# Kernel optimization log

Measured on AMD Instinct MI355X. Metric: run time of the kernel, lower is better.

The kernel has to match this reference:

```python
import jax, jax.numpy as jnp
import numpy as np

B, T, E, H, NH, L, R, K, N, P, HOR = 32, 16, 768, 1024, 16, 6, 8, 16, 100000, 9, 8
HD = H // NH


def _ln(x, g, b):
    m = jnp.mean(x, -1, keepdims=True)
    v = jnp.mean((x - m) ** 2, -1, keepdims=True)
    return (x - m) * jax.lax.rsqrt(v + 1e-5) * g + b


def _lora(x, W, A, Bm, b):
    # base linear + low-rank update: x W^T + (x A^T) B^T + b
    return x @ W.T + (x @ A.T) @ Bm.T + b


def setup_inputs() -> dict:
    key = jax.random.key(0)
    ks = iter(jax.random.split(key, 64))
    def rn(shape, s):
        return jax.random.normal(next(ks), shape, dtype=jnp.float32) * s
    d = {}
    d['history_img_emb'] = rn((B, T, E), 1.0)
    d['current_emb'] = rn((B, E), 1.0)
    d['goal_emb'] = rn((B, E), 1.0)
    d['subgoal_emb'] = rn((B, E), 1.0)
    d['beacon_emb'] = rn((B, E), 1.0)
    d['history_proprio'] = rn((B, T, P), 1.0)
    d['proprio'] = rn((B, P), 1.0)
    d['bank'] = rn((N, E), 1.0)
    d['hp_W'] = rn((H, E + P), 0.02); d['hp_b'] = jnp.zeros((H,), jnp.float32)
    d['ip_W'] = rn((H, E), 0.02); d['ip_b'] = jnp.zeros((H,), jnp.float32)
    d['pp_W'] = rn((H, P), 0.02); d['pp_b'] = jnp.zeros((H,), jnp.float32)
    d['plan_token'] = rn((1, 1, H), 0.02)
    d['ln1_g'] = jnp.ones((L, H), jnp.float32); d['ln1_b'] = jnp.zeros((L, H), jnp.float32)
    d['ln2_g'] = jnp.ones((L, H), jnp.float32); d['ln2_b'] = jnp.zeros((L, H), jnp.float32)
    for nm, o, i in (('q', H, H), ('k', H, H), ('v', H, H), ('o', H, H), ('f1', 4 * H, H), ('f2', H, 4 * H)):
        d[nm + 'W'] = rn((L, o, i), 0.02)
        d[nm + 'A'] = rn((L, R, i), 0.02)
        d[nm + 'B'] = rn((L, o, R), 0.02)
        d[nm + 'b'] = jnp.zeros((L, o), jnp.float32)
    d['fln_g'] = jnp.ones((H,), jnp.float32); d['fln_b'] = jnp.zeros((H,), jnp.float32)
    d['ah_W1'] = rn((H, H), 0.02); d['ah_b1'] = jnp.zeros((H,), jnp.float32)
    d['ah_W2'] = rn((3, H), 0.02); d['ah_b2'] = jnp.zeros((3,), jnp.float32)
    d['rh_W1'] = rn((H, H + 3), 0.02); d['rh_b1'] = jnp.zeros((H,), jnp.float32)
    d['rh_W2'] = rn((HOR * 3, H), 0.02); d['rh_b2'] = jnp.zeros((HOR * 3,), jnp.float32)
    d['sh_W'] = rn((1, H), 0.02); d['sh_b'] = jnp.zeros((1,), jnp.float32)
    return d


def reference(history_img_emb, current_emb, goal_emb, subgoal_emb, beacon_emb,
              history_proprio, proprio, bank,
              hp_W, hp_b, ip_W, ip_b, pp_W, pp_b, plan_token,
              ln1_g, ln1_b, ln2_g, ln2_b,
              qW, qA, qB, qb, kW, kA, kB, kb, vW, vA, vB, vb, oW, oA, oB, ob,
              f1W, f1A, f1B, f1b, f2W, f2A, f2B, f2b,
              fln_g, fln_b, ah_W1, ah_b1, ah_W2, ah_b2,
              rh_W1, rh_b1, rh_W2, rh_b2, sh_W, sh_b):
    # batched semantic-bank top-k retrieval (replaces the per-sample python loop)
    sims = current_emb @ bank.T                      # [B, N]
    scores, idx = jax.lax.top_k(sims, K)             # [B, K]
    sem = bank[idx] * scores[..., None]              # [B, K, E] gather + scale

    # multi-modal token fusion
    hist = jnp.concatenate([history_img_emb, history_proprio], -1) @ hp_W.T + hp_b  # [B, T, H]
    img = lambda e: e @ ip_W.T + ip_b
    goal_t = img(goal_emb)[:, None]
    sub_t = img(subgoal_emb)[:, None]
    bea_t = img(beacon_emb)[:, None]
    sem_t = img(sem)                                 # [B, K, H]
    prop_t = (proprio @ pp_W.T + pp_b)[:, None]
    plan_t = jnp.broadcast_to(plan_token, (B, 1, H))
    x = jnp.concatenate([plan_t, hist, goal_t, sub_t, bea_t, sem_t, prop_t], 1)  # [B, S=37, H]

    scale = 1.0 / np.sqrt(HD).astype(np.float32)
    for l in range(L):
        h = _ln(x, ln1_g[l], ln1_b[l])
        q = _lora(h, qW[l], qA[l], qB[l], qb[l]).reshape(B, -1, NH, HD)
        k = _lora(h, kW[l], kA[l], kB[l], kb[l]).reshape(B, -1, NH, HD)
        v = _lora(h, vW[l], vA[l], vB[l], vb[l]).reshape(B, -1, NH, HD)
        attn = jax.nn.softmax(jnp.einsum('bshd,bthd->bhst', q, k) * scale, axis=-1)
        out = jnp.einsum('bhst,bthd->bshd', attn, v).reshape(B, -1, H)
        x = x + _lora(out, oW[l], oA[l], oB[l], ob[l])
        h2 = _ln(x, ln2_g[l], ln2_b[l])
        x = x + _lora(jax.nn.gelu(_lora(h2, f1W[l], f1A[l], f1B[l], f1b[l]), approximate=False),
                      f2W[l], f2A[l], f2B[l], f2b[l])

    x = _ln(x, fln_g, fln_b)
    ps = x[:, 0]                                     # plan token state [B, H]
    anchor = jax.nn.gelu(ps @ ah_W1.T + ah_b1, approximate=False) @ ah_W2.T + ah_b2  # [B, 3]
    ref_in = jnp.concatenate([ps, anchor], -1)
    waypoints = (jax.nn.gelu(ref_in @ rh_W1.T + rh_b1, approximate=False) @ rh_W2.T + rh_b2).reshape(B, HOR, 3)
    stop_logit = (ps @ sh_W.T + sh_b)[:, 0]          # [B]
    return anchor, waypoints, stop_logit
```

## Files before the change

### kernel.cpp

```cpp
#include <hip/hip_runtime.h>
#include <float.h>
#include <math.h>

#define NB 100000
#define SEQ 37
#define NTOK 1184
#define TKCH 16

typedef __attribute__((ext_vector_type(8))) short short8;
typedef __attribute__((ext_vector_type(4))) float floatx4;

__device__ __forceinline__ short f2bf(float f) {
  union { float f; unsigned u; } x; x.f = f;
  unsigned r = x.u + 0x7fff + ((x.u >> 16) & 1);
  return (short)(r >> 16);
}

__device__ __forceinline__ float gelu_f(float v) {
  return 0.5f * v * (1.f + erff(v * 0.70710678118654752f));
}

__global__ __launch_bounds__(256) void wconv_all(const float* __restrict__ qW,
                                                 const float* __restrict__ kW,
                                                 const float* __restrict__ vW,
                                                 const float* __restrict__ oW,
                                                 const float* __restrict__ f1W,
                                                 const float* __restrict__ f2W,
                                                 short* __restrict__ wb) {
  const int l = blockIdx.x / 1536;
  const int t = blockIdx.x - l * 1536;
  const float* src; int Kd; size_t doff; int np, kc;
  if (t < 512) {
    const int w = t >> 7, ti = t & 127;
    const float* base = (w == 0) ? qW : (w == 1) ? kW : (w == 2) ? vW : oW;
    src = base + (size_t)l * 1024 * 1024;
    Kd = 1024; np = ti >> 4; kc = ti & 15;
    doff = (size_t)w * 1048576 + ((size_t)np * 16 + kc) * 8192;
  } else if (t < 1024) {
    const int ti = t - 512;
    src = f1W + (size_t)l * 4096 * 1024;
    Kd = 1024; np = ti >> 4; kc = ti & 15;
    doff = (size_t)4 * 1048576 + ((size_t)np * 16 + kc) * 8192;
  } else {
    const int ti = t - 1024;
    src = f2W + (size_t)l * 1024 * 4096;
    Kd = 4096; np = ti >> 6; kc = ti & 63;
    doff = (size_t)8 * 1048576 + ((size_t)np * 64 + kc) * 8192;
  }
  short* dst = wb + (size_t)l * 12 * 1048576 + doff;
  const float* sp = src + (size_t)(np * 128) * Kd + kc * 64;
  const int tid = threadIdx.x;
#pragma unroll
  for (int q = 0; q < 4; ++q) {
    const int d = q * 256 + tid;
    const int row = d >> 3, slot = d & 7;
    const int ss = slot ^ (row & 7);
    const float* s = sp + (size_t)row * Kd + ss * 8;
    const float4 u0 = *(const float4*)s;
    const float4 u1 = *(const float4*)(s + 4);
    short8 v;
    v[0] = f2bf(u0.x); v[1] = f2bf(u0.y); v[2] = f2bf(u0.z); v[3] = f2bf(u0.w);
    v[4] = f2bf(u1.x); v[5] = f2bf(u1.y); v[6] = f2bf(u1.z); v[7] = f2bf(u1.w);
    *(short8*)(dst + (size_t)d * 8) = v;
  }
}

__global__ __launch_bounds__(256) void wconv_embed(const float* __restrict__ hpW,
                                                   const float* __restrict__ ipW,
                                                   short* __restrict__ wbe) {
  const int t = blockIdx.x;
  const float* src; int Kd, np, kc; size_t doff;
  if (t < 104) { src = hpW; Kd = 777; np = t / 13; kc = t - np * 13; doff = (size_t)t * 8192; }
  else { const int ti = t - 104; src = ipW; Kd = 768; np = ti / 12; kc = ti - np * 12;
         doff = (size_t)t * 8192; }
  short* dst = wbe + doff;
  const int tid = threadIdx.x;
#pragma unroll
  for (int q = 0; q < 4; ++q) {
    const int d = q * 256 + tid;
    const int row = d >> 3, slot = d & 7;
    const int ss = slot ^ (row & 7);
    const int gk0 = kc * 64 + ss * 8;
    const float* s = src + (size_t)(np * 128 + row) * Kd;
    short8 v;
#pragma unroll
    for (int e = 0; e < 8; ++e) v[e] = (gk0 + e < Kd) ? f2bf(s[gk0 + e]) : (short)0;
    *(short8*)(dst + (size_t)d * 8) = v;
  }
}

__global__ __launch_bounds__(256) void gemm_bt(const float* __restrict__ A, int lda,
                                               const short* __restrict__ WT, size_t wzstride,
                                               const float* __restrict__ b0,
                                               const float* __restrict__ b1,
                                               const float* __restrict__ b2,
                                               const float* __restrict__ LT,
                                               const float* __restrict__ B0,
                                               const float* __restrict__ B1,
                                               const float* __restrict__ B2,
                                               float* __restrict__ C, size_t czstride,
                                               int ldc, int M, int K,
                                               int acc_flag, int gelu_flag,
                                               int ksn, float* __restrict__ part) {
  __shared__ short Al[2][64 * 64];
  __shared__ short Wl[2][128 * 64];
  const int z = blockIdx.z;
  const int kidx = (ksn > 1) ? z : 0;
  const float* bias = (ksn > 1 || z == 0) ? b0 : (z == 1) ? b1 : b2;
  const float* Bz = (ksn > 1 || z == 0) ? B0 : (z == 1) ? B1 : B2;
  if (ksn == 1) C += (size_t)z * czstride;
  const int nkc_tot = K >> 6;
  const int nkc = nkc_tot / ksn;
  const short* wt = WT + (size_t)((ksn > 1) ? 0 : z) * wzstride +
                    ((size_t)blockIdx.y * nkc_tot + (size_t)kidx * nkc) * 8192;
  const int tid = threadIdx.x;
  const int wid = tid >> 6, lane = tid & 63;
  const int wr = wid >> 1, wc = wid & 1;
  const int bm = blockIdx.x * 64, bn = blockIdx.y * 128;
  const int arow = tid >> 2;
  const int s0 = (tid & 3) * 2;

  floatx4 acc[2][4];
#pragma unroll
  for (int i = 0; i < 2; ++i)
#pragma unroll
    for (int j = 0; j < 4; ++j)
#pragma unroll
      for (int r = 0; r < 4; ++r) acc[i][j][r] = 0.f;

  const int ga = bm + arow;
  const bool aok = ga < M;
  const float* ap = A + (size_t)ga * lda + (size_t)kidx * nkc * 64;
  const int aswz = arow & 7;

  float4 ar[4];
  short8 wreg[4];

#define LOAD_A(kc_)                                                        \
  {                                                                        \
    _Pragma("unroll") for (int j = 0; j < 2; ++j) {                        \
      const int slot = s0 + j;                                             \
      if (aok) {                                                           \
        ar[j * 2] = *(const float4*)(ap + (kc_)*64 + slot * 8);            \
        ar[j * 2 + 1] = *(const float4*)(ap + (kc_)*64 + slot * 8 + 4);    \
      } else {                                                             \
        ar[j * 2] = make_float4(0.f, 0.f, 0.f, 0.f);                      \
        ar[j * 2 + 1] = make_float4(0.f, 0.f, 0.f, 0.f);                  \
      }                                                                    \
    }                                                                      \
  }
#define LOAD_W(kc_)                                                        \
  {                                                                        \
    _Pragma("unroll") for (int it = 0; it < 4; ++it)                       \
        wreg[it] = *(const short8*)(wt + (size_t)(kc_)*8192 + (it * 256 + tid) * 8); \
  }
#define WRITE_A(buf_)                                                      \
  {                                                                        \
    _Pragma("unroll") for (int j = 0; j < 2; ++j) {                        \
      const int slot = s0 + j;                                             \
      short8 s;                                                            \
      s[0] = f2bf(ar[j * 2].x); s[1] = f2bf(ar[j * 2].y);                  \
      s[2] = f2bf(ar[j * 2].z); s[3] = f2bf(ar[j * 2].w);                  \
      s[4] = f2bf(ar[j * 2 + 1].x); s[5] = f2bf(ar[j * 2 + 1].y);          \
      s[6] = f2bf(ar[j * 2 + 1].z); s[7] = f2bf(ar[j * 2 + 1].w);          \
      *(short8*)&Al[buf_][arow * 64 + ((slot ^ aswz) << 3)] = s;           \
    }                                                                      \
  }
#define WRITE_W(buf_)                                                      \
  {                                                                        \
    _Pragma("unroll") for (int it = 0; it < 4; ++it)                       \
        *(short8*)&Wl[buf_][(it * 256 + tid) * 8] = wreg[it];              \
  }

  LOAD_W(0) LOAD_A(0)
  WRITE_A(0) WRITE_W(0)
  __syncthreads();

  for (int t = 0; t < nkc; ++t) {
    const int cur = t & 1, nxt = cur ^ 1;
    const bool more = (t + 1 < nkc);
    if (more) { LOAD_W(t + 1) LOAD_A(t + 1) }
#pragma unroll
    for (int ks = 0; ks < 2; ++ks) {
      short8 af[2], wf[4];
#pragma unroll
      for (int i = 0; i < 2; ++i) {
        const int row = wr * 32 + i * 16 + (lane & 15);
        const int sa = (ks * 4 + (lane >> 4)) ^ (row & 7);
        af[i] = *(const short8*)&Al[cur][row * 64 + sa * 8];
      }
#pragma unroll
      for (int j = 0; j < 4; ++j) {
        const int col = wc * 64 + j * 16 + (lane & 15);
        const int sw2 = (ks * 4 + (lane >> 4)) ^ (col & 7);
        wf[j] = *(const short8*)&Wl[cur][col * 64 + sw2 * 8];
      }
#pragma unroll
      for (int i = 0; i < 2; ++i)
#pragma unroll
        for (int j = 0; j < 4; ++j)
          acc[i][j] = __builtin_amdgcn_mfma_f32_16x16x32_bf16(af[i], wf[j], acc[i][j], 0, 0, 0);
    }
    if (more) { WRITE_A(nxt) WRITE_W(nxt) }
    __syncthreads();
  }
#undef LOAD_A
#undef LOAD_W
#undef WRITE_A
#undef WRITE_W

  if (ksn > 1) {
#pragma unroll
    for (int i = 0; i < 2; ++i) {
      const int gm0 = bm + wr * 32 + i * 16 + (lane >> 4) * 4;
#pragma unroll
      for (int r = 0; r < 4; ++r) {
        const int gm = gm0 + r;
        if (gm >= M) continue;
#pragma unroll
        for (int j = 0; j < 4; ++j) {
          const int gn = bn + wc * 64 + j * 16 + (lane & 15);
          part[((size_t)kidx * M + gm) * ldc + gn] = acc[i][j][r];
        }
      }
    }
    return;
  }

  float br[4][8];
  if (LT) {
#pragma unroll
    for (int j = 0; j < 4; ++j) {
      const int gn = bn + wc * 64 + j * 16 + (lane & 15);
      const float4 u0 = *(const float4*)(Bz + (size_t)gn * 8);
      const float4 u1 = *(const float4*)(Bz + (size_t)gn * 8 + 4);
      br[j][0] = u0.x; br[j][1] = u0.y; br[j][2] = u0.z; br[j][3] = u0.w;
      br[j][4] = u1.x; br[j][5] = u1.y; br[j][6] = u1.z; br[j][7] = u1.w;
    }
  }
#pragma unroll
  for (int i = 0; i < 2; ++i) {
    const int gm0 = bm + wr * 32 + i * 16 + (lane >> 4) * 4;
#pragma unroll
    for (int r = 0; r < 4; ++r) {
      const int gm = gm0 + r;
      if (gm >= M) continue;
      float lt[8];
      if (LT) {
        const float4 t0 = *(const float4*)(LT + ((size_t)z * NTOK + gm) * 8);
        const float4 t1 = *(const float4*)(LT + ((size_t)z * NTOK + gm) * 8 + 4);
        lt[0] = t0.x; lt[1] = t0.y; lt[2] = t0.z; lt[3] = t0.w;
        lt[4] = t1.x; lt[5] = t1.y; lt[6] = t1.z; lt[7] = t1.w;
      }
#pragma unroll
      for (int j = 0; j < 4; ++j) {
        const int gn = bn + wc * 64 + j * 16 + (lane & 15);
        float o = acc[i][j][r] + bias[gn];
        if (LT)
          o += lt[0] * br[j][0] + lt[1] * br[j][1] + lt[2] * br[j][2] + lt[3] * br[j][3] +
               lt[4] * br[j][4] + lt[5] * br[j][5] + lt[6] * br[j][6] + lt[7] * br[j][7];
        const size_t off = (size_t)gm * ldc + gn;
        if (acc_flag) o += C[off];
        if (gelu_flag) o = gelu_f(o);
        C[off] = o;
      }
    }
  }
}

__global__ __launch_bounds__(256) void reduce_ks(const float* __restrict__ part,
                                                 const float* __restrict__ bias,
                                                 const float* __restrict__ LT,
                                                 const float* __restrict__ Bm,
                                                 float* __restrict__ X, int KS) {
  const int idx = blockIdx.x * 256 + threadIdx.x;
  if (idx >= NTOK * 1024) return;
  const int gm = idx >> 10, gn = idx & 1023;
  float s = 0.f;
  for (int h = 0; h < KS; ++h) s += part[(size_t)h * NTOK * 1024 + idx];
  const float* t = LT + (size_t)gm * 8;
  const float* bp = Bm + (size_t)gn * 8;
  s += t[0] * bp[0] + t[1] * bp[1] + t[2] * bp[2] + t[3] * bp[3] +
       t[4] * bp[4] + t[5] * bp[5] + t[6] * bp[6] + t[7] * bp[7];
  X[idx] += s + bias[gn];
}

__global__ __launch_bounds__(256) void gemm_sm2(const float* __restrict__ A, int lda,
                                                const float* __restrict__ W, int ldw,
                                                const float* __restrict__ bias,
                                                float* __restrict__ C, int ldc,
                                                float* __restrict__ part,
                                                int N, int K, int gelu_flag) {
  __shared__ float buf[8192];
  const int tid = threadIdx.x;
  const int col = tid >> 3, ksub = tid & 7;
  const int gcol = blockIdx.x * 32 + col;
  const int KS = gridDim.y, ky = blockIdx.y;
  const int kchunk = (((K + KS - 1) / KS) + 127) & ~127;
  const int kstart = ky * kchunk;
  const int kend = (kstart + kchunk < K) ? (kstart + kchunk) : K;
  const float* wp = W + (size_t)(gcol < N ? gcol : 0) * ldw;

  float acc[32];
#pragma unroll
  for (int m = 0; m < 32; ++m) acc[m] = 0.f;

  for (int kc = kstart; kc < kend; kc += 128) {
    __syncthreads();
#pragma unroll
    for (int q = 0; q < 4; ++q) {
      const int idx4 = q * 256 + tid;
      const int m = idx4 >> 5, j = (idx4 & 31) * 4;
      const int gk = kc + j;
      float4 v;
      if (gk + 3 < K) {
        v = *(const float4*)(A + (size_t)m * lda + gk);
      } else {
        v.x = (gk < K) ? A[(size_t)m * lda + gk] : 0.f;
        v.y = (gk + 1 < K) ? A[(size_t)m * lda + gk + 1] : 0.f;
        v.z = (gk + 2 < K) ? A[(size_t)m * lda + gk + 2] : 0.f;
        v.w = (gk + 3 < K) ? A[(size_t)m * lda + gk + 3] : 0.f;
      }
      *(float4*)&buf[m * 128 + j] = v;
    }
    __syncthreads();
#pragma unroll
    for (int kk = 0; kk < 4; ++kk) {
      const int j = kk * 32 + ksub * 4;
      const int gk = kc + j;
      float4 w4 = make_float4(0.f, 0.f, 0.f, 0.f);
      if (gcol < N && gk < K) {
        if (gk + 3 < K) {
          w4 = *(const float4*)(wp + gk);
        } else {
          w4.x = wp[gk];
          if (gk + 1 < K) w4.y = wp[gk + 1];
          if (gk + 2 < K) w4.z = wp[gk + 2];
        }
      }
#pragma unroll
      for (int m = 0; m < 32; ++m) {
        const float4 a4 = *(const float4*)&buf[m * 128 + j];
        acc[m] += a4.x * w4.x + a4.y * w4.y + a4.z * w4.z + a4.w * w4.w;
      }
    }
  }
  __syncthreads();
#pragma unroll
  for (int m = 0; m < 32; ++m) buf[m * 256 + ksub * 32 + col] = acc[m];
  __syncthreads();
#pragma unroll
  for (int g = 0; g < 4; ++g) {
    const int idx = g * 256 + tid;
    const int m = idx >> 5, c = idx & 31;
    float s = 0.f;
#pragma unroll
    for (int h = 0; h < 8; ++h) s += buf[m * 256 + h * 32 + c];
    const int gc = blockIdx.x * 32 + c;
    if (gc < N) {
      if (KS == 1) {
        float o = s + bias[gc];
        if (gelu_flag) o = gelu_f(o);
        C[(size_t)m * ldc + gc] = o;
      } else {
        part[((size_t)ky * 32 + m) * N + gc] = s;
      }
    }
  }
}

__global__ __launch_bounds__(256) void reduce_sm(const float* __restrict__ part,
                                                 const float* __restrict__ bias,
                                                 float* __restrict__ C, int ldc,
                                                 int N, int KS, int gelu_flag) {
  const int idx = blockIdx.x * 256 + threadIdx.x;
  if (idx >= 32 * N) return;
  const int m = idx / N, c = idx - m * N;
  float s = 0.f;
  for (int h = 0; h < KS; ++h) s += part[((size_t)h * 32 + m) * N + c];
  float o = s + bias[c];
  if (gelu_flag) o = gelu_f(o);
  C[(size_t)m * ldc + c] = o;
}

__global__ __launch_bounds__(256) void sims_kernel(const float* __restrict__ cur,
                                                   const float* __restrict__ bank,
                                                   float* __restrict__ sims) {
  __shared__ float Bs[32][132];
  __shared__ float Cs[32][36];
  const int tid = threadIdx.x;
  const int tx = tid & 7;
  const int ty = tid >> 3;
  const int n0 = blockIdx.x * 128;
  const int srow = tid >> 1;
  const int spart = tid & 1;
  const int cb = tid >> 3;
  const int ck = (tid & 7) * 4;

  float acc[4][4] = {{0.f,0.f,0.f,0.f},{0.f,0.f,0.f,0.f},
                     {0.f,0.f,0.f,0.f},{0.f,0.f,0.f,0.f}};

  const bool rok = (n0 + srow) < NB;
  const float* bp = bank + (size_t)(n0 + srow) * 768 + spart * 16;
  const float* cp = cur + (size_t)cb * 768 + ck;

  for (int kc = 0; kc < 768; kc += 32) {
    __syncthreads();
#pragma unroll
    for (int jj = 0; jj < 4; ++jj) {
      float4 v = rok ? *(const float4*)(bp + kc + jj * 4)
                     : make_float4(0.f, 0.f, 0.f, 0.f);
      const int kk = spart * 16 + jj * 4;
      Bs[kk + 0][srow] = v.x; Bs[kk + 1][srow] = v.y;
      Bs[kk + 2][srow] = v.z; Bs[kk + 3][srow] = v.w;
    }
    {
      float4 v = *(const float4*)(cp + kc);
      Cs[ck + 0][cb] = v.x; Cs[ck + 1][cb] = v.y;
      Cs[ck + 2][cb] = v.z; Cs[ck + 3][cb] = v.w;
    }
    __syncthreads();
#pragma unroll
    for (int kk = 0; kk < 32; ++kk) {
      float4 av = *(const float4*)&Bs[kk][ty * 4];
      float4 bv = *(const float4*)&Cs[kk][tx * 4];
      float a4[4] = {av.x, av.y, av.z, av.w};
      float b4[4] = {bv.x, bv.y, bv.z, bv.w};
#pragma unroll
      for (int i = 0; i < 4; ++i)
#pragma unroll
        for (int j = 0; j < 4; ++j) acc[i][j] += a4[i] * b4[j];
    }
  }
  const int n = n0 + ty * 4;
#pragma unroll
  for (int j = 0; j < 4; ++j) {
    const int b = tx * 4 + j;
    float4 o = make_float4(acc[0][j], acc[1][j], acc[2][j], acc[3][j]);
    if (n + 3 < NB) {
      *(float4*)(sims + (size_t)b * NB + n) = o;
    } else {
      float oo[4] = {o.x, o.y, o.z, o.w};
      for (int i = 0; i < 4; ++i)
        if (n + i < NB) sims[(size_t)b * NB + n + i] = oo[i];
    }
  }
}

__global__ __launch_bounds__(256) void topk_stage1(const float* __restrict__ sims,
                                                   float* __restrict__ cv,
                                                   int* __restrict__ ci) {
  __shared__ float ss[4096];
  __shared__ int si[4096];
  __shared__ float wv[4];
  __shared__ int wi[4];
  const int chunk = blockIdx.x, b = blockIdx.y, tid = threadIdx.x;
  const int start = chunk * (NB / TKCH), end = start + (NB / TKCH);
  float ls[16]; int li[16];
#pragma unroll
  for (int i = 0; i < 16; ++i) { ls[i] = -FLT_MAX; li[i] = 0x7fffffff; }
  const float* row = sims + (size_t)b * NB;
  float lmin = -FLT_MAX;
  for (int n = start + tid; n < end; n += 256) {
    float v = row[n];
    if (v > lmin) {
      int p = 15;
      while (p > 0 && ls[p - 1] < v) { ls[p] = ls[p - 1]; li[p] = li[p - 1]; --p; }
      ls[p] = v; li[p] = n;
      lmin = ls[15];
    }
  }
#pragma unroll
  for (int i = 0; i < 16; ++i) { ss[i * 256 + tid] = ls[i]; si[i * 256 + tid] = li[i]; }
  __syncthreads();
  for (int round = 0; round < 16; ++round) {
    float bv = -FLT_MAX; int bi = 0x7fffffff;
#pragma unroll
    for (int i = 0; i < 16; ++i) {
      float v = ss[i * 256 + tid]; int ix = si[i * 256 + tid];
      if (v > bv || (v == bv && ix < bi)) { bv = v; bi = ix; }
    }
#pragma unroll
    for (int s = 32; s; s >>= 1) {
      float ov = __shfl_down(bv, s); int oi = __shfl_down(bi, s);
      if (ov > bv || (ov == bv && oi < bi)) { bv = ov; bi = oi; }
    }
    if ((tid & 63) == 0) { wv[tid >> 6] = bv; wi[tid >> 6] = bi; }
    __syncthreads();
    if (tid == 0) {
      bv = wv[0]; bi = wi[0];
      for (int w = 1; w < 4; ++w)
        if (wv[w] > bv || (wv[w] == bv && wi[w] < bi)) { bv = wv[w]; bi = wi[w]; }
      cv[(b * TKCH + chunk) * 16 + round] = bv;
      ci[(b * TKCH + chunk) * 16 + round] = bi;
      wi[0] = bi;
    }
    __syncthreads();
    bi = wi[0];
#pragma unroll
    for (int i = 0; i < 16; ++i)
      if (si[i * 256 + tid] == bi) ss[i * 256 + tid] = -FLT_MAX;
    __syncthreads();
  }
}

__global__ __launch_bounds__(256) void topk_stage2(const float* __restrict__ cv,
                                                   const int* __restrict__ ci,
                                                   float* __restrict__ tks,
                                                   int* __restrict__ tki) {
  __shared__ float wv[4];
  __shared__ int wi[4];
  __shared__ int bw;
  const int b = blockIdx.x, tid = threadIdx.x;
  float val = cv[b * 256 + tid];
  int idx = ci[b * 256 + tid];
  for (int round = 0; round < 16; ++round) {
    float bv = val; int bi = idx;
#pragma unroll
    for (int s = 1; s < 64; s <<= 1) {
      float ov = __shfl_xor(bv, s); int oi = __shfl_xor(bi, s);
      if (ov > bv || (ov == bv && oi < bi)) { bv = ov; bi = oi; }
    }
    if ((tid & 63) == 0) { wv[tid >> 6] = bv; wi[tid >> 6] = bi; }
    __syncthreads();
    if (tid == 0) {
      bv = wv[0]; bi = wi[0];
      for (int w = 1; w < 4; ++w)
        if (wv[w] > bv || (wv[w] == bv && wi[w] < bi)) { bv = wv[w]; bi = wi[w]; }
      tks[b * 16 + round] = bv; tki[b * 16 + round] = bi;
      bw = bi;
    }
    __syncthreads();
    if (idx == bw) val = -FLT_MAX;
  }
}

__global__ void sem_kernel(const float* __restrict__ bank, const float* __restrict__ tks,
                           const int* __restrict__ tki, float* __restrict__ sem) {
  int slot = blockIdx.x;
  float s = tks[slot]; int idx = tki[slot];
  for (int i = threadIdx.x; i < 768; i += 256)
    sem[(size_t)slot * 768 + i] = bank[(size_t)idx * 768 + i] * s;
}

__global__ void build_hist_in(const float* __restrict__ img, const float* __restrict__ pr,
                              float* __restrict__ out) {
  int r = blockIdx.x;
  for (int i = threadIdx.x; i < 832; i += 256)
    out[(size_t)r * 832 + i] = (i < 768) ? img[(size_t)r * 768 + i]
                             : (i < 777) ? pr[r * 9 + (i - 768)] : 0.f;
}

__global__ void build_img_in(const float* __restrict__ goal, const float* __restrict__ sub,
                             const float* __restrict__ bea, const float* __restrict__ sem,
                             float* __restrict__ out) {
  int r = blockIdx.x;
  const float* src = (r < 32) ? goal + (size_t)r * 768
                   : (r < 64) ? sub + (size_t)(r - 32) * 768
                   : (r < 96) ? bea + (size_t)(r - 64) * 768
                              : sem + (size_t)(r - 96) * 768;
  for (int i = threadIdx.x; i < 768; i += 256) out[(size_t)r * 768 + i] = src[i];
}

__global__ void assemble_x(const float* __restrict__ th, const float* __restrict__ ti,
                           const float* __restrict__ tp, const float* __restrict__ plan,
                           float* __restrict__ x) {
  int r = blockIdx.x;
  int b = r / SEQ, tok = r - b * SEQ;
  const float* src;
  if (tok == 0) src = plan;
  else if (tok <= 16) src = th + (size_t)(b * 16 + tok - 1) * 1024;
  else if (tok <= 19) src = ti + (size_t)((tok - 17) * 32 + b) * 1024;
  else if (tok <= 35) src = ti + (size_t)(96 + b * 16 + (tok - 20)) * 1024;
  else src = tp + (size_t)b * 1024;
  for (int i = threadIdx.x; i < 1024; i += 256) x[(size_t)r * 1024 + i] = src[i];
}

__global__ void build_ref(const float* __restrict__ ps, const float* __restrict__ anc,
                          float* __restrict__ ref) {
  int b = blockIdx.x;
  for (int i = threadIdx.x; i < 1027; i += 256)
    ref[(size_t)b * 1027 + i] = (i < 1024) ? ps[(size_t)b * 1024 + i] : anc[b * 3 + (i - 1024)];
}

__device__ __forceinline__ float block_sum256(float v, float* red) {
#pragma unroll
  for (int s = 32; s; s >>= 1) v += __shfl_down(v, s);
  if ((threadIdx.x & 63) == 0) red[threadIdx.x >> 6] = v;
  __syncthreads();
  float tot = red[0] + red[1] + red[2] + red[3];
  __syncthreads();
  return tot;
}

__global__ __launch_bounds__(256) void ln_kernel(const float* __restrict__ in, int in_stride,
                                                 float* __restrict__ out,
                                                 const float* __restrict__ g,
                                                 const float* __restrict__ bt) {
  __shared__ float red[4];
  const float* xr = in + (size_t)blockIdx.x * in_stride;
  const int tid = threadIdx.x;
  float v[4];
#pragma unroll
  for (int i = 0; i < 4; ++i) v[i] = xr[tid + 256 * i];
  float mean = block_sum256(v[0] + v[1] + v[2] + v[3], red) * (1.f / 1024.f);
  float sq = 0.f;
#pragma unroll
  for (int i = 0; i < 4; ++i) { float d = v[i] - mean; sq += d * d; }
  float var = block_sum256(sq, red) * (1.f / 1024.f);
  float inv = rsqrtf(var + 1e-5f);
  float* orow = out + (size_t)blockIdx.x * 1024;
#pragma unroll
  for (int i = 0; i < 4; ++i) {
    int c = tid + 256 * i;
    orow[c] = (v[i] - mean) * inv * g[c] + bt[c];
  }
}

__global__ __launch_bounds__(256) void lora_down(const float* __restrict__ h,
                                                 const float* __restrict__ A0,
                                                 const float* __restrict__ A1,
                                                 const float* __restrict__ A2,
                                                 float* __restrict__ lt, int K) {
  __shared__ float red[4][8];
  const int m = blockIdx.x, z = blockIdx.y;
  const int tid = threadIdx.x, wave = tid >> 6, lane = tid & 63;
  const float* A = (z == 0) ? A0 : (z == 1) ? A1 : A2;
  float p[8] = {0.f, 0.f, 0.f, 0.f, 0.f, 0.f, 0.f, 0.f};
  for (int kk = tid; kk < K; kk += 256) {
    float hv = h[(size_t)m * K + kk];
#pragma unroll
    for (int r = 0; r < 8; ++r) p[r] += hv * A[r * K + kk];
  }
#pragma unroll
  for (int s = 1; s < 64; s <<= 1) {
#pragma unroll
    for (int r = 0; r < 8; ++r) p[r] += __shfl_xor(p[r], s);
  }
  if (lane == 0) {
#pragma unroll
    for (int r = 0; r < 8; ++r) red[wave][r] = p[r];
  }
  __syncthreads();
  if (tid < 8)
    lt[((size_t)z * NTOK + m) * 8 + tid] =
        red[0][tid] + red[1][tid] + red[2][tid] + red[3][tid];
}

__global__ __launch_bounds__(256) void attn_kernel(const float* __restrict__ q,
                                                   const float* __restrict__ k,
                                                   const float* __restrict__ v,
                                                   float* __restrict__ ao) {
  __shared__ float qs[SEQ * 64], ks[SEQ * 64], vs[SEQ * 64], sc[SEQ * 40];
  const int head = blockIdx.x, b = blockIdx.y, tid = threadIdx.x;
  const size_t base = ((size_t)b * SEQ) * 1024 + head * 64;
  for (int i = tid; i < SEQ * 64; i += 256) {
    int s = i >> 6, d = i & 63;
    size_t off = base + (size_t)s * 1024 + d;
    qs[i] = q[off]; ks[i] = k[off]; vs[i] = v[off];
  }
  __syncthreads();
  for (int p = tid; p < SEQ * SEQ; p += 256) {
    int s = p / SEQ, t = p - s * SEQ;
    float acc = 0.f;
#pragma unroll 16
    for (int d = 0; d < 64; ++d) acc += qs[s * 64 + d] * ks[t * 64 + d];
    sc[s * 40 + t] = acc * 0.125f;
  }
  __syncthreads();
  if (tid < SEQ) {
    float m = -FLT_MAX;
    for (int t = 0; t < SEQ; ++t) m = fmaxf(m, sc[tid * 40 + t]);
    float sum = 0.f;
    for (int t = 0; t < SEQ; ++t) { float e = expf(sc[tid * 40 + t] - m); sc[tid * 40 + t] = e; sum += e; }
    float inv = 1.f / sum;
    for (int t = 0; t < SEQ; ++t) sc[tid * 40 + t] *= inv;
  }
  __syncthreads();
  for (int i = tid; i < SEQ * 64; i += 256) {
    int s = i >> 6, d = i & 63;
    float acc = 0.f;
    for (int t = 0; t < SEQ; ++t) acc += sc[s * 40 + t] * vs[t * 64 + d];
    ao[base + (size_t)s * 1024 + d] = acc;
  }
}

extern "C" void kernel_launch(void* const* d_in, const int* in_sizes, int n_in,
                              void* d_out, int out_size, void* d_ws, size_t ws_size,
                              hipStream_t stream) {
  const float* hist_img = (const float*)d_in[0];
  const float* cur      = (const float*)d_in[1];
  const float* goal     = (const float*)d_in[2];
  const float* sub      = (const float*)d_in[3];
  const float* bea      = (const float*)d_in[4];
  const float* hist_pr  = (const float*)d_in[5];
  const float* prop     = (const float*)d_in[6];
  const float* bank     = (const float*)d_in[7];
  const float* hpW = (const float*)d_in[8];  const float* hpb = (const float*)d_in[9];
  const float* ipW = (const float*)d_in[10]; const float* ipb = (const float*)d_in[11];
  const float* ppW = (const float*)d_in[12]; const float* ppb = (const float*)d_in[13];
  const float* plan = (const float*)d_in[14];
  const float* ln1g = (const float*)d_in[15]; const float* ln1b = (const float*)d_in[16];
  const float* ln2g = (const float*)d_in[17]; const float* ln2b = (const float*)d_in[18];
  const float* qW = (const float*)d_in[19]; const float* qA = (const float*)d_in[20];
  const float* qB = (const float*)d_in[21]; const float* qb = (const float*)d_in[22];
  const float* kW = (const float*)d_in[23]; const float* kA = (const float*)d_in[24];
  const float* kB = (const float*)d_in[25]; const float* kb = (const float*)d_in[26];
  const float* vW = (const float*)d_in[27]; const float* vA = (const float*)d_in[28];
  const float* vB = (const float*)d_in[29]; const float* vb = (const float*)d_in[30];
  const float* oW = (const float*)d_in[31]; const float* oA = (const float*)d_in[32];
  const float* oB = (const float*)d_in[33]; const float* ob = (const float*)d_in[34];
  const float* f1W = (const float*)d_in[35]; const float* f1A = (const float*)d_in[36];
  const float* f1B = (const float*)d_in[37]; const float* f1b = (const float*)d_in[38];
  const float* f2W = (const float*)d_in[39]; const float* f2A = (const float*)d_in[40];
  const float* f2B = (const float*)d_in[41]; const float* f2b = (const float*)d_in[42];
  const float* flng = (const float*)d_in[43]; const float* flnb = (const float*)d_in[44];
  const float* ahW1 = (const float*)d_in[45]; const float* ahb1 = (const float*)d_in[46];
  const float* ahW2 = (const float*)d_in[47]; const float* ahb2 = (const float*)d_in[48];
  const float* rhW1 = (const float*)d_in[49]; const float* rhb1 = (const float*)d_in[50];
  const float* rhW2 = (const float*)d_in[51]; const float* rhb2 = (const float*)d_in[52];
  const float* shW = (const float*)d_in[53]; const float* shb = (const float*)d_in[54];
  float* out = (float*)d_out;

  float* ws  = (float*)d_ws;
  float* F1O = ws;
  float* SIMS = ws;
  float* X   = F1O + (size_t)NTOK * 4096;
  float* Hb  = X  + (size_t)NTOK * 1024;
  float* Qb  = Hb + (size_t)NTOK * 1024;
  float* Kb  = Qb + (size_t)NTOK * 1024;
  float* Vb  = Kb + (size_t)NTOK * 1024;
  float* AOb = Vb + (size_t)NTOK * 1024;
  float* LT  = AOb + (size_t)NTOK * 1024;
  float* SEM = LT + (size_t)3 * NTOK * 8;
  float* HIN = SEM + (size_t)512 * 768;
  float* TKS = HIN + (size_t)512 * 832;
  int*   TKI = (int*)(TKS + 512);
  float* PS  = TKS + 1024;
  float* HH  = PS + 32 * 1024;
  float* REF = HH + 32 * 1024;
  float* CV  = REF + 32 * 1027;
  int*   CI  = (int*)(CV + 32 * 256);
  float* PART = (float*)(CI + 32 * 256);
  float* PF2 = PART + 8 * 32 * 1024;
  short* WB  = (short*)(PF2 + (size_t)4 * NTOK * 1024);
  short* WBE = WB + (size_t)6 * 12 * 1048576;

  const size_t czs = (size_t)NTOK * 1024;
  const size_t WM = 1048576;
  const size_t WL = 12 * WM;

  auto gemms = [&](const float* A, int lda, const float* W, int ldw, const float* bias,
                   float* C, int ldc, int N, int K, int geluf, int KS) {
    gemm_sm2<<<dim3((N + 31) / 32, KS), 256, 0, stream>>>(A, lda, W, ldw, bias,
                                                          C, ldc, PART, N, K, geluf);
    if (KS > 1)
      reduce_sm<<<(32 * N + 255) / 256, 256, 0, stream>>>(PART, bias, C, ldc, N, KS, geluf);
  };

  wconv_all<<<6 * 1536, 256, 0, stream>>>(qW, kW, vW, oW, f1W, f2W, WB);
  wconv_embed<<<200, 256, 0, stream>>>(hpW, ipW, WBE);

  sims_kernel<<<(NB + 127) / 128, 256, 0, stream>>>(cur, bank, SIMS);
  topk_stage1<<<dim3(TKCH, 32), 256, 0, stream>>>(SIMS, CV, CI);
  topk_stage2<<<32, 256, 0, stream>>>(CV, CI, TKS, TKI);
  sem_kernel<<<512, 256, 0, stream>>>(bank, TKS, TKI, SEM);

  build_hist_in<<<512, 256, 0, stream>>>(hist_img, hist_pr, HIN);
  build_img_in<<<608, 256, 0, stream>>>(goal, sub, bea, SEM, AOb);
  gemm_bt<<<dim3(8, 8, 1), 256, 0, stream>>>(
      HIN, 832, WBE, 0, hpb, hpb, hpb,
      nullptr, nullptr, nullptr, nullptr, Qb, 0, 1024, 512, 832, 0, 0, 1, nullptr);
  gemm_bt<<<dim3(10, 8, 1), 256, 0, stream>>>(
      AOb, 768, WBE + (size_t)104 * 8192, 0, ipb, ipb, ipb,
      nullptr, nullptr, nullptr, nullptr, Kb, 0, 1024, 608, 768, 0, 0, 1, nullptr);
  gemms(prop, 9, ppW, 9, ppb, Vb, 1024, 1024, 9, 0, 1);
  assemble_x<<<NTOK, 256, 0, stream>>>(Qb, Kb, Vb, plan, X);

  const int mblk = (NTOK + 63) / 64;
  for (int l = 0; l < 6; ++l) {
    const size_t aO = (size_t)l * 8 * 1024, bO = (size_t)l * 1024 * 8,
                 biO = (size_t)l * 1024;
    const size_t a4O = (size_t)l * 8 * 4096, b4O = (size_t)l * 4096 * 8,
                 bi4O = (size_t)l * 4096;
    const short* WBl = WB + (size_t)l * WL;
    ln_kernel<<<NTOK, 256, 0, stream>>>(X, 1024, Hb, ln1g + biO, ln1b + biO);
    lora_down<<<dim3(NTOK, 3), 256, 0, stream>>>(Hb, qA + aO, kA + aO, vA + aO, LT, 1024);
    gemm_bt<<<dim3(mblk, 8, 3), 256, 0, stream>>>(
        Hb, 1024, WBl, WM, qb + biO, kb + biO, vb + biO,
        LT, qB + bO, kB + bO, vB + bO, Qb, czs, 1024, NTOK, 1024, 0, 0, 1, nullptr);
    attn_kernel<<<dim3(16, 32), 256, 0, stream>>>(Qb, Kb, Vb, AOb);
    lora_down<<<dim3(NTOK, 1), 256, 0, stream>>>(AOb, oA + aO, oA + aO, oA + aO, LT, 1024);
    gemm_bt<<<dim3(mblk, 8, 2), 256, 0, stream>>>(
        AOb, 1024, WBl + 3 * WM, 0, ob + biO, ob + biO, ob + biO,
        nullptr, nullptr, nullptr, nullptr, nullptr, 0, 1024, NTOK, 1024, 0, 0, 2, PF2);
    reduce_ks<<<(NTOK * 1024 + 255) / 256, 256, 0, stream>>>(PF2, ob + biO, LT,
                                                             oB + bO, X, 2);
    ln_kernel<<<NTOK, 256, 0, stream>>>(X, 1024, Hb, ln2g + biO, ln2b + biO);
    lora_down<<<dim3(NTOK, 1), 256, 0, stream>>>(Hb, f1A + aO, f1A + aO, f1A + aO, LT, 1024);
    gemm_bt<<<dim3(mblk, 32, 1), 256, 0, stream>>>(
        Hb, 1024, WBl + 4 * WM, 0, f1b + bi4O, f1b + bi4O, f1b + bi4O,
        LT, f1B + b4O, f1B + b4O, f1B + b4O, F1O, 0, 4096, NTOK, 1024, 0, 1, 1, nullptr);
    lora_down<<<dim3(NTOK, 1), 256, 0, stream>>>(F1O, f2A + a4O, f2A + a4O, f2A + a4O, LT, 4096);
    gemm_bt<<<dim3(mblk, 8, 4), 256, 0, stream>>>(
        F1O, 4096, WBl + 8 * WM, 0, f2b + biO, f2b + biO, f2b + biO,
        nullptr, nullptr, nullptr, nullptr, nullptr, 0, 1024, NTOK, 4096, 0, 0, 4, PF2);
    reduce_ks<<<(NTOK * 1024 + 255) / 256, 256, 0, stream>>>(PF2, f2b + biO, LT,
                                                             f2B + bO, X, 4);
  }

  ln_kernel<<<32, 256, 0, stream>>>(X, SEQ * 1024, PS, flng, flnb);
  gemms(PS, 1024, ahW1, 1024, ahb1, HH, 1024, 1024, 1024, 1, 8);
  gemms(HH, 1024, ahW2, 1024, ahb2, out, 3, 3, 1024, 0, 8);
  build_ref<<<32, 256, 0, stream>>>(PS, out, REF);
  gemms(REF, 1027, rhW1, 1027, rhb1, HH, 1024, 1024, 1027, 1, 8);
  gemms(HH, 1024, rhW2, 1024, rhb2, out + 96, 24, 24, 1024, 0, 8);
  gemms(PS, 1024, shW, 1024, shb, out + 864, 1, 1, 1024, 0, 8);
}
```

Measured before the change: 1.725 ms.

## Convert weights to bf16 inside GEMM loads and fuse LoRA-down into layernorm

Removes the separate weight pre-conversion kernels. The GEMM now loads fp32 weights directly, converts them to bf16 and writes them swizzled into shared memory, which avoids one full read and write pass over all layer weights per call. The LoRA down-projections for q/k/v and f1 are also computed inside the layernorm kernel, removing two lora_down launches per layer and a reread of the normalized activations. In exchange, the GEMM reads twice as many weight bytes per tile and does the conversion work on the critical path inside the main loop.

```diff
diff --git a/kernel.cpp b/kernel.cpp
--- a/kernel.cpp
+++ b/kernel.cpp
@@ -20,77 +20,11 @@
   return 0.5f * v * (1.f + erff(v * 0.70710678118654752f));
 }
 
-__global__ __launch_bounds__(256) void wconv_all(const float* __restrict__ qW,
-                                                 const float* __restrict__ kW,
-                                                 const float* __restrict__ vW,
-                                                 const float* __restrict__ oW,
-                                                 const float* __restrict__ f1W,
-                                                 const float* __restrict__ f2W,
-                                                 short* __restrict__ wb) {
-  const int l = blockIdx.x / 1536;
-  const int t = blockIdx.x - l * 1536;
-  const float* src; int Kd; size_t doff; int np, kc;
-  if (t < 512) {
-    const int w = t >> 7, ti = t & 127;
-    const float* base = (w == 0) ? qW : (w == 1) ? kW : (w == 2) ? vW : oW;
-    src = base + (size_t)l * 1024 * 1024;
-    Kd = 1024; np = ti >> 4; kc = ti & 15;
-    doff = (size_t)w * 1048576 + ((size_t)np * 16 + kc) * 8192;
-  } else if (t < 1024) {
-    const int ti = t - 512;
-    src = f1W + (size_t)l * 4096 * 1024;
-    Kd = 1024; np = ti >> 4; kc = ti & 15;
-    doff = (size_t)4 * 1048576 + ((size_t)np * 16 + kc) * 8192;
-  } else {
-    const int ti = t - 1024;
-    src = f2W + (size_t)l * 1024 * 4096;
-    Kd = 4096; np = ti >> 6; kc = ti & 63;
-    doff = (size_t)8 * 1048576 + ((size_t)np * 64 + kc) * 8192;
-  }
-  short* dst = wb + (size_t)l * 12 * 1048576 + doff;
-  const float* sp = src + (size_t)(np * 128) * Kd + kc * 64;
-  const int tid = threadIdx.x;
-#pragma unroll
-  for (int q = 0; q < 4; ++q) {
-    const int d = q * 256 + tid;
-    const int row = d >> 3, slot = d & 7;
-    const int ss = slot ^ (row & 7);
-    const float* s = sp + (size_t)row * Kd + ss * 8;
-    const float4 u0 = *(const float4*)s;
-    const float4 u1 = *(const float4*)(s + 4);
-    short8 v;
-    v[0] = f2bf(u0.x); v[1] = f2bf(u0.y); v[2] = f2bf(u0.z); v[3] = f2bf(u0.w);
-    v[4] = f2bf(u1.x); v[5] = f2bf(u1.y); v[6] = f2bf(u1.z); v[7] = f2bf(u1.w);
-    *(short8*)(dst + (size_t)d * 8) = v;
-  }
-}
-
-__global__ __launch_bounds__(256) void wconv_embed(const float* __restrict__ hpW,
-                                                   const float* __restrict__ ipW,
-                                                   short* __restrict__ wbe) {
-  const int t = blockIdx.x;
-  const float* src; int Kd, np, kc; size_t doff;
-  if (t < 104) { src = hpW; Kd = 777; np = t / 13; kc = t - np * 13; doff = (size_t)t * 8192; }
-  else { const int ti = t - 104; src = ipW; Kd = 768; np = ti / 12; kc = ti - np * 12;
-         doff = (size_t)t * 8192; }
-  short* dst = wbe + doff;
-  const int tid = threadIdx.x;
-#pragma unroll
-  for (int q = 0; q < 4; ++q) {
-    const int d = q * 256 + tid;
-    const int row = d >> 3, slot = d & 7;
-    const int ss = slot ^ (row & 7);
-    const int gk0 = kc * 64 + ss * 8;
-    const float* s = src + (size_t)(np * 128 + row) * Kd;
-    short8 v;
-#pragma unroll
-    for (int e = 0; e < 8; ++e) v[e] = (gk0 + e < Kd) ? f2bf(s[gk0 + e]) : (short)0;
-    *(short8*)(dst + (size_t)d * 8) = v;
-  }
-}
-
 __global__ __launch_bounds__(256) void gemm_bt(const float* __restrict__ A, int lda,
-                                               const short* __restrict__ WT, size_t wzstride,
+                                               const float* __restrict__ W0,
+                                               const float* __restrict__ W1,
+                                               const float* __restrict__ W2,
+                                               int ldw, int Kreal,
                                                const float* __restrict__ b0,
                                                const float* __restrict__ b1,
                                                const float* __restrict__ b2,
@@ -106,19 +40,19 @@
   __shared__ short Wl[2][128 * 64];
   const int z = blockIdx.z;
   const int kidx = (ksn > 1) ? z : 0;
+  const float* Wz = (ksn > 1 || z == 0) ? W0 : (z == 1) ? W1 : W2;
   const float* bias = (ksn > 1 || z == 0) ? b0 : (z == 1) ? b1 : b2;
   const float* Bz = (ksn > 1 || z == 0) ? B0 : (z == 1) ? B1 : B2;
   if (ksn == 1) C += (size_t)z * czstride;
-  const int nkc_tot = K >> 6;
-  const int nkc = nkc_tot / ksn;
-  const short* wt = WT + (size_t)((ksn > 1) ? 0 : z) * wzstride +
-                    ((size_t)blockIdx.y * nkc_tot + (size_t)kidx * nkc) * 8192;
+  const int nkc = (K >> 6) / ksn;
+  const int kofs = kidx * nkc * 64;
+  const int krel = Kreal - kofs;
   const int tid = threadIdx.x;
   const int wid = tid >> 6, lane = tid & 63;
   const int wr = wid >> 1, wc = wid & 1;
   const int bm = blockIdx.x * 64, bn = blockIdx.y * 128;
-  const int arow = tid >> 2;
-  const int s0 = (tid & 3) * 2;
+  const int arow = tid >> 2, s0 = (tid & 3) * 2;
+  const int wrow = tid >> 1, ws0 = (tid & 1) * 4;
 
   floatx4 acc[2][4];
 #pragma unroll
@@ -130,11 +64,12 @@
 
   const int ga = bm + arow;
   const bool aok = ga < M;
-  const float* ap = A + (size_t)ga * lda + (size_t)kidx * nkc * 64;
-  const int aswz = arow & 7;
+  const float* ap = A + (size_t)ga * lda + kofs;
+  const float* wp = Wz + (size_t)(bn + wrow) * ldw + kofs;
+  const int aswz = arow & 7, wswz = wrow & 7;
 
   float4 ar[4];
-  short8 wreg[4];
+  float4 wreg[8];
 
 #define LOAD_A(kc_)                                                        \
   {                                                                        \
@@ -151,8 +86,20 @@
   }
 #define LOAD_W(kc_)                                                        \
   {                                                                        \
-    _Pragma("unroll") for (int it = 0; it < 4; ++it)                       \
-        wreg[it] = *(const short8*)(wt + (size_t)(kc_)*8192 + (it * 256 + tid) * 8); \
+    _Pragma("unroll") for (int j = 0; j < 4; ++j) {                        \
+      const int slot = ws0 + j;                                            \
+      const int kg = (kc_)*64 + slot * 8;                                  \
+      if (kg + 7 < krel) {                                                 \
+        wreg[j * 2] = *(const float4*)(wp + kg);                           \
+        wreg[j * 2 + 1] = *(const float4*)(wp + kg + 4);                   \
+      } else {                                                             \
+        float t[8];                                                        \
+        _Pragma("unroll") for (int e = 0; e < 8; ++e)                      \
+            t[e] = (kg + e < krel) ? wp[kg + e] : 0.f;                     \
+        wreg[j * 2] = make_float4(t[0], t[1], t[2], t[3]);                 \
+        wreg[j * 2 + 1] = make_float4(t[4], t[5], t[6], t[7]);             \
+      }                                                                    \
+    }                                                                      \
   }
 #define WRITE_A(buf_)                                                      \
   {                                                                        \
@@ -168,8 +115,15 @@
   }
 #define WRITE_W(buf_)                                                      \
   {                                                                        \
-    _Pragma("unroll") for (int it = 0; it < 4; ++it)                       \
-        *(short8*)&Wl[buf_][(it * 256 + tid) * 8] = wreg[it];              \
+    _Pragma("unroll") for (int j = 0; j < 4; ++j) {                        \
+      const int slot = ws0 + j;                                            \
+      short8 s;                                                            \
+      s[0] = f2bf(wreg[j * 2].x); s[1] = f2bf(wreg[j * 2].y);              \
+      s[2] = f2bf(wreg[j * 2].z); s[3] = f2bf(wreg[j * 2].w);              \
+      s[4] = f2bf(wreg[j * 2 + 1].x); s[5] = f2bf(wreg[j * 2 + 1].y);      \
+      s[6] = f2bf(wreg[j * 2 + 1].z); s[7] = f2bf(wreg[j * 2 + 1].w);      \
+      *(short8*)&Wl[buf_][wrow * 64 + ((slot ^ wswz) << 3)] = s;           \
+    }                                                                      \
   }
 
   LOAD_W(0) LOAD_A(0)
@@ -596,10 +550,16 @@
 __global__ __launch_bounds__(256) void ln_kernel(const float* __restrict__ in, int in_stride,
                                                  float* __restrict__ out,
                                                  const float* __restrict__ g,
-                                                 const float* __restrict__ bt) {
+                                                 const float* __restrict__ bt,
+                                                 const float* __restrict__ A0,
+                                                 const float* __restrict__ A1,
+                                                 const float* __restrict__ A2,
+                                                 int nz, float* __restrict__ lt) {
   __shared__ float red[4];
+  __shared__ float red2[4][8];
   const float* xr = in + (size_t)blockIdx.x * in_stride;
   const int tid = threadIdx.x;
+  const int wave = tid >> 6, lane = tid & 63;
   float v[4];
 #pragma unroll
   for (int i = 0; i < 4; ++i) v[i] = xr[tid + 256 * i];
@@ -610,10 +570,37 @@
   float var = block_sum256(sq, red) * (1.f / 1024.f);
   float inv = rsqrtf(var + 1e-5f);
   float* orow = out + (size_t)blockIdx.x * 1024;
+  float nv[4];
 #pragma unroll
   for (int i = 0; i < 4; ++i) {
     int c = tid + 256 * i;
-    orow[c] = (v[i] - mean) * inv * g[c] + bt[c];
+    nv[i] = (v[i] - mean) * inv * g[c] + bt[c];
+    orow[c] = nv[i];
+  }
+  for (int z = 0; z < nz; ++z) {
+    const float* Am = (z == 0) ? A0 : (z == 1) ? A1 : A2;
+    float p[8];
+#pragma unroll
+    for (int r = 0; r < 8; ++r) {
+      float s = 0.f;
+#pragma unroll
+      for (int i = 0; i < 4; ++i) s += nv[i] * Am[r * 1024 + tid + 256 * i];
+      p[r] = s;
+    }
+#pragma unroll
+    for (int sh = 1; sh < 64; sh <<= 1) {
+#pragma unroll
+      for (int r = 0; r < 8; ++r) p[r] += __shfl_xor(p[r], sh);
+    }
+    if (lane == 0) {
+#pragma unroll
+      for (int r = 0; r < 8; ++r) red2[wave][r] = p[r];
+    }
+    __syncthreads();
+    if (tid < 8)
+      lt[((size_t)z * NTOK + blockIdx.x) * 8 + tid] =
+          red2[0][tid] + red2[1][tid] + red2[2][tid] + red2[3][tid];
+    __syncthreads();
   }
 }
 
@@ -743,12 +730,8 @@
   int*   CI  = (int*)(CV + 32 * 256);
   float* PART = (float*)(CI + 32 * 256);
   float* PF2 = PART + 8 * 32 * 1024;
-  short* WB  = (short*)(PF2 + (size_t)4 * NTOK * 1024);
-  short* WBE = WB + (size_t)6 * 12 * 1048576;
 
   const size_t czs = (size_t)NTOK * 1024;
-  const size_t WM = 1048576;
-  const size_t WL = 12 * WM;
 
   auto gemms = [&](const float* A, int lda, const float* W, int ldw, const float* bias,
                    float* C, int ldc, int N, int K, int geluf, int KS) {
@@ -758,9 +741,6 @@
       reduce_sm<<<(32 * N + 255) / 256, 256, 0, stream>>>(PART, bias, C, ldc, N, KS, geluf);
   };
 
-  wconv_all<<<6 * 1536, 256, 0, stream>>>(qW, kW, vW, oW, f1W, f2W, WB);
-  wconv_embed<<<200, 256, 0, stream>>>(hpW, ipW, WBE);
-
   sims_kernel<<<(NB + 127) / 128, 256, 0, stream>>>(cur, bank, SIMS);
   topk_stage1<<<dim3(TKCH, 32), 256, 0, stream>>>(SIMS, CV, CI);
   topk_stage2<<<32, 256, 0, stream>>>(CV, CI, TKS, TKI);
@@ -769,47 +749,49 @@
   build_hist_in<<<512, 256, 0, stream>>>(hist_img, hist_pr, HIN);
   build_img_in<<<608, 256, 0, stream>>>(goal, sub, bea, SEM, AOb);
   gemm_bt<<<dim3(8, 8, 1), 256, 0, stream>>>(
-      HIN, 832, WBE, 0, hpb, hpb, hpb,
+      HIN, 832, hpW, hpW, hpW, 777, 777, hpb, hpb, hpb,
       nullptr, nullptr, nullptr, nullptr, Qb, 0, 1024, 512, 832, 0, 0, 1, nullptr);
   gemm_bt<<<dim3(10, 8, 1), 256, 0, stream>>>(
-      AOb, 768, WBE + (size_t)104 * 8192, 0, ipb, ipb, ipb,
+      AOb, 768, ipW, ipW, ipW, 768, 768, ipb, ipb, ipb,
       nullptr, nullptr, nullptr, nullptr, Kb, 0, 1024, 608, 768, 0, 0, 1, nullptr);
   gemms(prop, 9, ppW, 9, ppb, Vb, 1024, 1024, 9, 0, 1);
   assemble_x<<<NTOK, 256, 0, stream>>>(Qb, Kb, Vb, plan, X);
 
   const int mblk = (NTOK + 63) / 64;
   for (int l = 0; l < 6; ++l) {
-    const size_t aO = (size_t)l * 8 * 1024, bO = (size_t)l * 1024 * 8,
-                 biO = (size_t)l * 1024;
-    const size_t a4O = (size_t)l * 8 * 4096, b4O = (size_t)l * 4096 * 8,
-                 bi4O = (size_t)l * 4096;
-    const short* WBl = WB + (size_t)l * WL;
-    ln_kernel<<<NTOK, 256, 0, stream>>>(X, 1024, Hb, ln1g + biO, ln1b + biO);
-    lora_down<<<dim3(NTOK, 3), 256, 0, stream>>>(Hb, qA + aO, kA + aO, vA + aO, LT, 1024);
+    const size_t wO = (size_t)l * 1024 * 1024, aO = (size_t)l * 8 * 1024,
+                 bO = (size_t)l * 1024 * 8, biO = (size_t)l * 1024;
+    const size_t w4O = (size_t)l * 4096 * 1024, a4O = (size_t)l * 8 * 4096,
+                 b4O = (size_t)l * 4096 * 8, bi4O = (size_t)l * 4096;
+    ln_kernel<<<NTOK, 256, 0, stream>>>(X, 1024, Hb, ln1g + biO, ln1b + biO,
+                                        qA + aO, kA + aO, vA + aO, 3, LT);
     gemm_bt<<<dim3(mblk, 8, 3), 256, 0, stream>>>(
-        Hb, 1024, WBl, WM, qb + biO, kb + biO, vb + biO,
+        Hb, 1024, qW + wO, kW + wO, vW + wO, 1024, 1024, qb + biO, kb + biO, vb + biO,
         LT, qB + bO, kB + bO, vB + bO, Qb, czs, 1024, NTOK, 1024, 0, 0, 1, nullptr);
     attn_kernel<<<dim3(16, 32), 256, 0, stream>>>(Qb, Kb, Vb, AOb);
     lora_down<<<dim3(NTOK, 1), 256, 0, stream>>>(AOb, oA + aO, oA + aO, oA + aO, LT, 1024);
     gemm_bt<<<dim3(mblk, 8, 2), 256, 0, stream>>>(
-        AOb, 1024, WBl + 3 * WM, 0, ob + biO, ob + biO, ob + biO,
+        AOb, 1024, oW + wO, oW + wO, oW + wO, 1024, 1024, ob + biO, ob + biO, ob + biO,
         nullptr, nullptr, nullptr, nullptr, nullptr, 0, 1024, NTOK, 1024, 0, 0, 2, PF2);
     reduce_ks<<<(NTOK * 1024 + 255) / 256, 256, 0, stream>>>(PF2, ob + biO, LT,
                                                              oB + bO, X, 2);
-    ln_kernel<<<NTOK, 256, 0, stream>>>(X, 1024, Hb, ln2g + biO, ln2b + biO);
-    lora_down<<<dim3(NTOK, 1), 256, 0, stream>>>(Hb, f1A + aO, f1A + aO, f1A + aO, LT, 1024);
+    ln_kernel<<<NTOK, 256, 0, stream>>>(X, 1024, Hb, ln2g + biO, ln2b + biO,
+                                        f1A + aO, f1A + aO, f1A + aO, 1, LT);
     gemm_bt<<<dim3(mblk, 32, 1), 256, 0, stream>>>(
-        Hb, 1024, WBl + 4 * WM, 0, f1b + bi4O, f1b + bi4O, f1b + bi4O,
+        Hb, 1024, f1W + w4O, f1W + w4O, f1W + w4O, 1024, 1024,
+        f1b + bi4O, f1b + bi4O, f1b + bi4O,
         LT, f1B + b4O, f1B + b4O, f1B + b4O, F1O, 0, 4096, NTOK, 1024, 0, 1, 1, nullptr);
     lora_down<<<dim3(NTOK, 1), 256, 0, stream>>>(F1O, f2A + a4O, f2A + a4O, f2A + a4O, LT, 4096);
     gemm_bt<<<dim3(mblk, 8, 4), 256, 0, stream>>>(
-        F1O, 4096, WBl + 8 * WM, 0, f2b + biO, f2b + biO, f2b + biO,
+        F1O, 4096, f2W + w4O, f2W + w4O, f2W + w4O, 4096, 4096,
+        f2b + biO, f2b + biO, f2b + biO,
         nullptr, nullptr, nullptr, nullptr, nullptr, 0, 1024, NTOK, 4096, 0, 0, 4, PF2);
     reduce_ks<<<(NTOK * 1024 + 255) / 256, 256, 0, stream>>>(PF2, f2b + biO, LT,
                                                              f2B + bO, X, 4);
   }
 
-  ln_kernel<<<32, 256, 0, stream>>>(X, SEQ * 1024, PS, flng, flnb);
+  ln_kernel<<<32, 256, 0, stream>>>(X, SEQ * 1024, PS, flng, flnb,
+                                    nullptr, nullptr, nullptr, 0, nullptr);
   gemms(PS, 1024, ahW1, 1024, ahb1, HH, 1024, 1024, 1024, 1, 8);
   gemms(HH, 1024, ahW2, 1024, ahb2, out, 3, 3, 1024, 0, 8);
   build_ref<<<32, 256, 0, stream>>>(PS, out, REF);
```

New measurement: 2.417 ms. 1.4x slower.
